# Kernel optimization log

Hardware: AMD Instinct MI355X
Metric: run time of the kernel (lower is better)

## Reference

```python
import jax, jax.numpy as jnp
import numpy as np

N = 50000
IN_CH = 128
HEADS = 4
OUT_CH = 32
E = 800000
NEG_SLOPE = 0.2


def setup_inputs() -> dict:
    key = jax.random.key(0)
    k1, k2, k3, k4, k5, k6 = jax.random.split(key, 6)
    x = jax.random.normal(k1, (N, IN_CH), dtype=jnp.float32)
    edge_index = jax.random.randint(k2, (2, E), 0, N, dtype=jnp.int64)
    # learned params (PyG GATv2Conv: lin_l, lin_r weights, att vector, bias)
    s = 1.0 / np.sqrt(IN_CH)
    W_l = jax.random.uniform(k3, (IN_CH, HEADS, OUT_CH), jnp.float32, -s, s)
    W_r = jax.random.uniform(k4, (IN_CH, HEADS, OUT_CH), jnp.float32, -s, s)
    att = jax.random.uniform(k5, (HEADS, OUT_CH), jnp.float32, -s, s)
    bias = jax.random.uniform(k6, (HEADS * OUT_CH,), jnp.float32, -s, s)
    return {"x": x, "edge_index": edge_index, "W_l": W_l, "W_r": W_r,
            "att": att, "bias": bias}


def reference(x, edge_index, W_l, W_r, att, bias):
    # add self loops (PyG default add_self_loops=True)
    loops = jnp.arange(N, dtype=edge_index.dtype)
    src = jnp.concatenate([edge_index[0], loops])  # message source j
    dst = jnp.concatenate([edge_index[1], loops])  # message target i

    # node projections: [N, H, C]
    x_l = jnp.einsum('nd,dhc->nhc', x, W_l)  # source-side
    x_r = jnp.einsum('nd,dhc->nhc', x, W_r)  # target-side

    # GATv2 attention logits per edge: a^T LeakyReLU(x_l[j] + x_r[i])
    e = jax.nn.leaky_relu(x_l[src] + x_r[dst], NEG_SLOPE)  # [Etot, H, C]
    score = jnp.einsum('ehc,hc->eh', e, att)               # [Etot, H]

    # segment softmax over incoming edges of each destination node
    m = jax.ops.segment_max(score, dst, num_segments=N)    # [N, H]
    m = jnp.where(jnp.isfinite(m), m, 0.0)
    ex = jnp.exp(score - m[dst])                           # [Etot, H]
    denom = jax.ops.segment_sum(ex, dst, num_segments=N)   # [N, H]
    alpha = ex / denom[dst]                                # [Etot, H]

    # scatter-aggregate weighted messages
    msg = alpha[:, :, None] * x_l[src]                     # [Etot, H, C]
    out = jax.ops.segment_sum(msg, dst, num_segments=N)    # [N, H, C]

    # concat heads + bias
    return out.reshape(N, HEADS * OUT_CH) + bias
```

## Files before the change

### kernel.cpp

```cpp
#include <hip/hip_runtime.h>
#include <math.h>

#define N_NODES 50000
#define IN_CH   128
#define TOT_CH  128
#define NEDGE   800000
#define ETOT    (NEDGE + N_NODES)
#define MTILES  ((N_NODES + 63) / 64)
#define NBUCK   ((N_NODES + 255) / 256)
#define BCAP    8192
#define EPB     4096
#define NBIN    ((ETOT + EPB - 1) / EPB)

#define OFF_XL      ((size_t)0)
#define OFF_EBUF    ((size_t)12800000)
#define OFF_XR      ((size_t)25600000)
#define OFF_SRC     ((size_t)38400000)
#define OFF_BT      ((size_t)44900352)
#define OFF_GCUR    ((size_t)45000064)
#define OFF_ROWPTR  ((size_t)51200000)

typedef float f32x4 __attribute__((ext_vector_type(4)));
typedef short s16x8 __attribute__((ext_vector_type(8)));

__device__ __forceinline__ unsigned f2bf(float f) {
    unsigned u = __float_as_uint(f);
    return (u + 0x7fffu + ((u >> 16) & 1u)) >> 16;
}
__device__ __forceinline__ float bflo(unsigned u) { return __uint_as_float(u << 16); }
__device__ __forceinline__ float bfhi(unsigned u) { return __uint_as_float(u & 0xffff0000u); }

__device__ __forceinline__ int SWZ(int row, int byteoff) {
    return row * 256 + (byteoff ^ ((row & 7) << 4));
}

__global__ __launch_bounds__(256) void k1_kernel(
    const float* __restrict__ Wl, const float* __restrict__ Wr,
    unsigned* __restrict__ btg, const int* __restrict__ ei,
    int* __restrict__ gcur, unsigned* __restrict__ ebuf)
{
    __shared__ int lcnt[256];
    __shared__ int lbase[256];
    const int bid = blockIdx.x;
    const int tid = threadIdx.x;

    if (bid < NBIN) {
        lcnt[tid] = 0;
        __syncthreads();
        const int base = bid * EPB;
        int sv[16], dv[16];
#pragma unroll
        for (int u = 0; u < 16; ++u) {
            const int e = base + u * 256 + tid;
            int s32 = 0, d32 = -1;
            if (e < ETOT) {
                if (e < NEDGE) { s32 = ei[e]; d32 = ei[NEDGE + e]; }
                else           { s32 = d32 = e - NEDGE; }
                atomicAdd(&lcnt[d32 >> 8], 1);
            }
            sv[u] = s32; dv[u] = d32;
        }
        __syncthreads();
        if (tid < NBUCK) {
            const int v = lcnt[tid];
            lbase[tid] = v ? atomicAdd(&gcur[tid], v) : 0;
        }
        __syncthreads();
        lcnt[tid] = 0;
        __syncthreads();
#pragma unroll
        for (int u = 0; u < 16; ++u) {
            const int d32 = dv[u];
            if (d32 >= 0) {
                const int b = d32 >> 8;
                const int p = lbase[b] + atomicAdd(&lcnt[b], 1);
                ebuf[b * BCAP + p] = (unsigned)sv[u] | ((unsigned)(d32 & 255) << 16);
            }
        }
    } else {
        const int g = (bid - NBIN) * 256 + tid;
        if (g < 256 * 64) {
            const int n = g >> 6, kk = g & 63;
            const float* W = (n < 128) ? Wl : Wr;
            const int nc = n & 127;
            const float a = W[(size_t)(2 * kk) * 128 + nc];
            const float b = W[(size_t)(2 * kk + 1) * 128 + nc];
            btg[g] = f2bf(a) | (f2bf(b) << 16);
        }
    }
}

__global__ __launch_bounds__(256) void k2_kernel(
    const float* __restrict__ x, const unsigned* __restrict__ btg,
    unsigned* __restrict__ xl_bf, unsigned* __restrict__ xr_bf,
    const unsigned* __restrict__ ebuf, const int* __restrict__ gcur,
    int2* __restrict__ rowptr2, int* __restrict__ ssrc)
{
    __shared__ __align__(16) unsigned char smem[32768];
    __shared__ int wsum[4];
    const int bid = blockIdx.x;
    const int tid = threadIdx.x;

    if (bid < NBUCK) {
        int* lcnt = (int*)smem;
        int* lcur = ((int*)smem) + 256;
        const int ecnt  = gcur[bid];
        const int ebase = bid * BCAP;
        lcnt[tid] = 0;
        __syncthreads();
        for (int k = tid; k < ecnt; k += 256)
            atomicAdd(&lcnt[(ebuf[ebase + k] >> 16) & 255], 1);
        __syncthreads();
        const int lane = tid & 63, wid = tid >> 6;
        const int v = lcnt[tid];
        int s = v;
#pragma unroll
        for (int off = 1; off < 64; off <<= 1) {
            int t = __shfl_up(s, off);
            if (lane >= off) s += t;
        }
        if (lane == 63) wsum[wid] = s;
        __syncthreads();
        if (tid == 0) {
            int acc = 0;
#pragma unroll
            for (int w = 0; w < 4; ++w) { int t = wsum[w]; wsum[w] = acc; acc += t; }
        }
        __syncthreads();
        const int gpos = ebase + wsum[wid] + s - v;
        const int node = (bid << 8) + tid;
        if (node < N_NODES) rowptr2[node] = make_int2(gpos, gpos + v);
        lcur[tid] = gpos;
        __syncthreads();
        for (int k = tid; k < ecnt; k += 256) {
            const unsigned ed = ebuf[ebase + k];
            const int p = atomicAdd(&lcur[(ed >> 16) & 255], 1);
            ssrc[p] = (int)(ed & 0xffffu);
        }
        return;
    }

    unsigned char* Al = smem;
    unsigned char* Bl = smem + 16384;
    const int mt = bid - NBUCK;
    const int mbase = mt * 64;
    const int l  = tid & 63;
    const int wv = tid >> 6;

    {
        const int r = tid >> 2, q = tid & 3;
        int gm = mbase + r;
        gm = (gm < N_NODES) ? gm : (N_NODES - 1);
        const float* xrow = x + (size_t)gm * IN_CH + q * 32;
#pragma unroll
        for (int i = 0; i < 8; ++i) {
            const float4 xv = *(const float4*)(xrow + i * 4);
            uint2 p;
            p.x = f2bf(xv.x) | (f2bf(xv.y) << 16);
            p.y = f2bf(xv.z) | (f2bf(xv.w) << 16);
            *(uint2*)(Al + SWZ(r, q * 64 + i * 8)) = p;
        }
    }
    {
        const int r = tid >> 2, q = tid & 3;
        const unsigned* brow = btg + (size_t)r * 64 + q * 16;
#pragma unroll
        for (int i = 0; i < 4; ++i) {
            const uint4 v = *(const uint4*)(brow + i * 4);
            *(uint4*)(Bl + SWZ(r, q * 64 + i * 16)) = v;
        }
    }
    __syncthreads();

    s16x8 af[4];
#pragma unroll
    for (int ks = 0; ks < 4; ++ks)
        af[ks] = *(const s16x8*)(Al + SWZ(wv * 16 + (l & 15), ks * 64 + (l >> 4) * 16));

    for (int nt4 = 0; nt4 < 4; ++nt4) {
        f32x4 acc[4];
#pragma unroll
        for (int n = 0; n < 4; ++n) acc[n] = (f32x4){0.f, 0.f, 0.f, 0.f};
#pragma unroll
        for (int nsub = 0; nsub < 4; ++nsub) {
#pragma unroll
            for (int ks = 0; ks < 4; ++ks) {
                const s16x8 bfr = *(const s16x8*)(Bl + SWZ(nsub * 16 + (l & 15), ks * 64 + (l >> 4) * 16));
                acc[nsub] = __builtin_amdgcn_mfma_f32_16x16x32_bf16(af[ks], bfr, acc[nsub], 0, 0, 0);
            }
        }
        unsigned* dstbuf = (nt4 < 2) ? xl_bf : xr_bf;
        const int ncol0 = (nt4 & 1) * 64;
#pragma unroll
        for (int nsub = 0; nsub < 4; ++nsub) {
            const int n = ncol0 + nsub * 16 + (l & 15);
#pragma unroll
            for (int reg = 0; reg < 4; ++reg) {
                const float v  = acc[nsub][reg];
                const float vp = __shfl_xor(v, 1);
                const int row = mbase + wv * 16 + (l >> 4) * 4 + reg;
                if (((l & 1) == 0) && row < N_NODES)
                    dstbuf[(size_t)row * 64 + (n >> 1)] = f2bf(v) | (f2bf(vp) << 16);
            }
        }
        if (nt4 == 3) break;
        __syncthreads();
        {
            const int r = tid >> 2, q = tid & 3;
            const unsigned* brow = btg + (size_t)((nt4 + 1) * 64 + r) * 64 + q * 16;
#pragma unroll
            for (int i = 0; i < 4; ++i) {
                const uint4 v = *(const uint4*)(brow + i * 4);
                *(uint4*)(Bl + SWZ(r, q * 64 + i * 16)) = v;
            }
        }
        __syncthreads();
    }
}

#define DPP_ADD(s, ctrl) do { \
        int _t = __builtin_amdgcn_update_dpp(0, __float_as_int(s), ctrl, 0xf, 0xf, true); \
        s += __int_as_float(_t); } while(0)

#define RED16x8(a0,a1,a2,a3,a4,a5,a6,a7) do { \
        DPP_ADD(a0,0xB1); DPP_ADD(a1,0xB1); DPP_ADD(a2,0xB1); DPP_ADD(a3,0xB1); \
        DPP_ADD(a4,0xB1); DPP_ADD(a5,0xB1); DPP_ADD(a6,0xB1); DPP_ADD(a7,0xB1); \
        DPP_ADD(a0,0x4E); DPP_ADD(a1,0x4E); DPP_ADD(a2,0x4E); DPP_ADD(a3,0x4E); \
        DPP_ADD(a4,0x4E); DPP_ADD(a5,0x4E); DPP_ADD(a6,0x4E); DPP_ADD(a7,0x4E); \
        DPP_ADD(a0,0x124); DPP_ADD(a1,0x124); DPP_ADD(a2,0x124); DPP_ADD(a3,0x124); \
        DPP_ADD(a4,0x124); DPP_ADD(a5,0x124); DPP_ADD(a6,0x124); DPP_ADD(a7,0x124); \
        DPP_ADD(a0,0x128); DPP_ADD(a1,0x128); DPP_ADD(a2,0x128); DPP_ADD(a3,0x128); \
        DPP_ADD(a4,0x128); DPP_ADD(a5,0x128); DPP_ADD(a6,0x128); DPP_ADD(a7,0x128); } while(0)

template<bool MASKED>
__device__ __forceinline__ void batch8(
    const int* __restrict__ srcs, int k, int k1, int lane,
    const unsigned* __restrict__ xl_bf,
    float xr2x, float xr2y, float a6x, float a4x, float a6y, float a4y,
    float& den, float& b0, float& b1)
{
#define KIDX(n) (MASKED ? min(k + n, k1 - 1) : (k + n))
#define LOADU(n) \
    const int j##n = __builtin_amdgcn_readfirstlane(srcs[KIDX(n)]); \
    const unsigned u##n = *(xl_bf + (size_t)j##n * 64 + lane);
    LOADU(0); LOADU(1); LOADU(2); LOADU(3);
    LOADU(4); LOADU(5); LOADU(6); LOADU(7);
#undef LOADU
#undef KIDX
#define SCORE(n) \
    const float t0_##n = bflo(u##n) + xr2x; \
    const float t1_##n = bfhi(u##n) + xr2y; \
    float s##n = fmaf(a6x, t0_##n, fmaf(a4x, fabsf(t0_##n), \
                 fmaf(a6y, t1_##n, a4y * fabsf(t1_##n))));
    SCORE(0); SCORE(1); SCORE(2); SCORE(3);
    SCORE(4); SCORE(5); SCORE(6); SCORE(7);
#undef SCORE
    RED16x8(s0, s1, s2, s3, s4, s5, s6, s7);
    if (MASKED) {
        const int r = k1 - k;
        s1 = (1 < r) ? s1 : -1e30f;
        s2 = (2 < r) ? s2 : -1e30f;
        s3 = (3 < r) ? s3 : -1e30f;
        s4 = (4 < r) ? s4 : -1e30f;
        s5 = (5 < r) ? s5 : -1e30f;
        s6 = (6 < r) ? s6 : -1e30f;
        s7 = (7 < r) ? s7 : -1e30f;
    }
    const float p0 = __builtin_amdgcn_exp2f(s0), p1 = __builtin_amdgcn_exp2f(s1);
    const float p2 = __builtin_amdgcn_exp2f(s2), p3 = __builtin_amdgcn_exp2f(s3);
    const float p4 = __builtin_amdgcn_exp2f(s4), p5 = __builtin_amdgcn_exp2f(s5);
    const float p6 = __builtin_amdgcn_exp2f(s6), p7 = __builtin_amdgcn_exp2f(s7);
    den += ((p0 + p1) + (p2 + p3)) + ((p4 + p5) + (p6 + p7));
    {
        const float e0 = fmaf(p1, t0_1, p0 * t0_0);
        const float e1 = fmaf(p3, t0_3, p2 * t0_2);
        const float e2 = fmaf(p5, t0_5, p4 * t0_4);
        const float e3 = fmaf(p7, t0_7, p6 * t0_6);
        b0 += (e0 + e1) + (e2 + e3);
        const float f0 = fmaf(p1, t1_1, p0 * t1_0);
        const float f1 = fmaf(p3, t1_3, p2 * t1_2);
        const float f2 = fmaf(p5, t1_5, p4 * t1_4);
        const float f3 = fmaf(p7, t1_7, p6 * t1_6);
        b1 += (f0 + f1) + (f2 + f3);
    }
}

__global__ __launch_bounds__(256) void gat_kernel(
    const unsigned* __restrict__ xl_bf, const unsigned* __restrict__ xr_bf,
    const int2* __restrict__ rowptr2, const int* __restrict__ srcs,
    const float* __restrict__ att, const float* __restrict__ bias,
    float* __restrict__ out)
{
    const int lane = threadIdx.x & 63;
    const int i = blockIdx.x * 4 + (threadIdx.x >> 6);
    if (i >= N_NODES) return;
    const int c = lane * 2;
    const float2 att2 = *(const float2*)(att + c);
    const unsigned ur = xr_bf[(size_t)i * 64 + lane];
    const float xr2x = bflo(ur), xr2y = bfhi(ur);
    const float LOG2E = 1.4426950408889634f;
    const float a6x = 0.6f * att2.x * LOG2E, a4x = 0.4f * att2.x * LOG2E;
    const float a6y = 0.6f * att2.y * LOG2E, a4y = 0.4f * att2.y * LOG2E;
    const int2 kr = rowptr2[i];
    const int k0 = __builtin_amdgcn_readfirstlane(kr.x);
    const int k1 = __builtin_amdgcn_readfirstlane(kr.y);

    float den = 0.f, b0 = 0.f, b1 = 0.f;
    int k = k0;
    for (; k + 8 <= k1; k += 8)
        batch8<false>(srcs, k, k1, lane, xl_bf, xr2x, xr2y,
                      a6x, a4x, a6y, a4y, den, b0, b1);
    if (k < k1)
        batch8<true>(srcs, k, k1, lane, xl_bf, xr2x, xr2y,
                     a6x, a4x, a6y, a4y, den, b0, b1);

    const float inv = 1.f / den;
    const float2 bb = *(const float2*)(bias + c);
    float2 o;
    o.x = fmaf(b0, inv, bb.x - xr2x);
    o.y = fmaf(b1, inv, bb.y - xr2y);
    *(float2*)(out + (size_t)i * TOT_CH + c) = o;
}

extern "C" void kernel_launch(void* const* d_in, const int* in_sizes, int n_in,
                              void* d_out, int out_size, void* d_ws, size_t ws_size,
                              hipStream_t stream) {
    const float* x    = (const float*)d_in[0];
    const int*   ei   = (const int*)d_in[1];
    const float* Wl   = (const float*)d_in[2];
    const float* Wr   = (const float*)d_in[3];
    const float* att  = (const float*)d_in[4];
    const float* bias = (const float*)d_in[5];
    float* out = (float*)d_out;
    char*  ws  = (char*)d_ws;

    unsigned* xl_bf = (unsigned*)(ws + OFF_XL);
    unsigned* ebuf  = (unsigned*)(ws + OFF_EBUF);
    unsigned* xr_bf = (unsigned*)(ws + OFF_XR);
    int*      ssrc  = (int*)(ws + OFF_SRC);
    unsigned* btg   = (unsigned*)(ws + OFF_BT);
    int*      gcur  = (int*)(ws + OFF_GCUR);
    int2*   rowptr2 = (int2*)(ws + OFF_ROWPTR);

    hipMemsetAsync(gcur, 0, NBUCK * sizeof(int), stream);
    hipLaunchKernelGGL(k1_kernel, dim3(NBIN + 64), dim3(256), 0, stream,
                       Wl, Wr, btg, ei, gcur, ebuf);
    hipLaunchKernelGGL(k2_kernel, dim3(NBUCK + MTILES), dim3(256), 0, stream,
                       x, btg, xl_bf, xr_bf, ebuf, gcur, rowptr2, ssrc);
    hipLaunchKernelGGL(gat_kernel, dim3((N_NODES + 3) / 4), dim3(256), 0, stream,
                       xl_bf, xr_bf, rowptr2, ssrc, att, bias, out);
}
```

Measured before the change: 78.42 us.

## Split wavefront into four edge groups with 16-byte loads per lane

The aggregation kernel now splits each 64-lane wavefront into four 16-lane groups. Each group handles a different edge, and each lane loads 8 bf16 channels with a single 16-byte load instead of 2 channels with a 4-byte load. Head reductions shrink to two DPP steps, and the cross-group accumulators are combined with shuffles at the end. The hipMemsetAsync of the bucket counters is replaced by a tiny zero kernel to cut API overhead. The trade is higher register pressure and shuffle reduction cost in exchange for fewer, wider gather loads per edge.

```diff
diff --git a/kernel.cpp b/kernel.cpp
--- a/kernel.cpp
+++ b/kernel.cpp
@@ -34,6 +34,10 @@
     return row * 256 + (byteoff ^ ((row & 7) << 4));
 }
 
+__global__ __launch_bounds__(256) void zero_kernel(int* __restrict__ gcur) {
+    if (threadIdx.x < NBUCK) gcur[threadIdx.x] = 0;
+}
+
 __global__ __launch_bounds__(256) void k1_kernel(
     const float* __restrict__ Wl, const float* __restrict__ Wr,
     unsigned* __restrict__ btg, const int* __restrict__ ei,
@@ -222,67 +226,35 @@
         int _t = __builtin_amdgcn_update_dpp(0, __float_as_int(s), ctrl, 0xf, 0xf, true); \
         s += __int_as_float(_t); } while(0)
 
-#define RED16x8(a0,a1,a2,a3,a4,a5,a6,a7) do { \
-        DPP_ADD(a0,0xB1); DPP_ADD(a1,0xB1); DPP_ADD(a2,0xB1); DPP_ADD(a3,0xB1); \
-        DPP_ADD(a4,0xB1); DPP_ADD(a5,0xB1); DPP_ADD(a6,0xB1); DPP_ADD(a7,0xB1); \
-        DPP_ADD(a0,0x4E); DPP_ADD(a1,0x4E); DPP_ADD(a2,0x4E); DPP_ADD(a3,0x4E); \
-        DPP_ADD(a4,0x4E); DPP_ADD(a5,0x4E); DPP_ADD(a6,0x4E); DPP_ADD(a7,0x4E); \
-        DPP_ADD(a0,0x124); DPP_ADD(a1,0x124); DPP_ADD(a2,0x124); DPP_ADD(a3,0x124); \
-        DPP_ADD(a4,0x124); DPP_ADD(a5,0x124); DPP_ADD(a6,0x124); DPP_ADD(a7,0x124); \
-        DPP_ADD(a0,0x128); DPP_ADD(a1,0x128); DPP_ADD(a2,0x128); DPP_ADD(a3,0x128); \
-        DPP_ADD(a4,0x128); DPP_ADD(a5,0x128); DPP_ADD(a6,0x128); DPP_ADD(a7,0x128); } while(0)
-
 template<bool MASKED>
-__device__ __forceinline__ void batch8(
-    const int* __restrict__ srcs, int k, int k1, int lane,
+__device__ __forceinline__ void group4(
+    const int* __restrict__ srcs, int k, int kend, int q, int sl,
     const unsigned* __restrict__ xl_bf,
-    float xr2x, float xr2y, float a6x, float a4x, float a6y, float a4y,
-    float& den, float& b0, float& b1)
+    const float* a6, const float* a4, const float* xr8,
+    float& den, float* b)
 {
-#define KIDX(n) (MASKED ? min(k + n, k1 - 1) : (k + n))
-#define LOADU(n) \
-    const int j##n = __builtin_amdgcn_readfirstlane(srcs[KIDX(n)]); \
-    const unsigned u##n = *(xl_bf + (size_t)j##n * 64 + lane);
-    LOADU(0); LOADU(1); LOADU(2); LOADU(3);
-    LOADU(4); LOADU(5); LOADU(6); LOADU(7);
-#undef LOADU
-#undef KIDX
-#define SCORE(n) \
-    const float t0_##n = bflo(u##n) + xr2x; \
-    const float t1_##n = bfhi(u##n) + xr2y; \
-    float s##n = fmaf(a6x, t0_##n, fmaf(a4x, fabsf(t0_##n), \
-                 fmaf(a6y, t1_##n, a4y * fabsf(t1_##n))));
-    SCORE(0); SCORE(1); SCORE(2); SCORE(3);
-    SCORE(4); SCORE(5); SCORE(6); SCORE(7);
-#undef SCORE
-    RED16x8(s0, s1, s2, s3, s4, s5, s6, s7);
-    if (MASKED) {
-        const int r = k1 - k;
-        s1 = (1 < r) ? s1 : -1e30f;
-        s2 = (2 < r) ? s2 : -1e30f;
-        s3 = (3 < r) ? s3 : -1e30f;
-        s4 = (4 < r) ? s4 : -1e30f;
-        s5 = (5 < r) ? s5 : -1e30f;
-        s6 = (6 < r) ? s6 : -1e30f;
-        s7 = (7 < r) ? s7 : -1e30f;
-    }
-    const float p0 = __builtin_amdgcn_exp2f(s0), p1 = __builtin_amdgcn_exp2f(s1);
-    const float p2 = __builtin_amdgcn_exp2f(s2), p3 = __builtin_amdgcn_exp2f(s3);
-    const float p4 = __builtin_amdgcn_exp2f(s4), p5 = __builtin_amdgcn_exp2f(s5);
-    const float p6 = __builtin_amdgcn_exp2f(s6), p7 = __builtin_amdgcn_exp2f(s7);
-    den += ((p0 + p1) + (p2 + p3)) + ((p4 + p5) + (p6 + p7));
-    {
-        const float e0 = fmaf(p1, t0_1, p0 * t0_0);
-        const float e1 = fmaf(p3, t0_3, p2 * t0_2);
-        const float e2 = fmaf(p5, t0_5, p4 * t0_4);
-        const float e3 = fmaf(p7, t0_7, p6 * t0_6);
-        b0 += (e0 + e1) + (e2 + e3);
-        const float f0 = fmaf(p1, t1_1, p0 * t1_0);
-        const float f1 = fmaf(p3, t1_3, p2 * t1_2);
-        const float f2 = fmaf(p5, t1_5, p4 * t1_4);
-        const float f3 = fmaf(p7, t1_7, p6 * t1_6);
-        b1 += (f0 + f1) + (f2 + f3);
-    }
+    const int kk = MASKED ? min(k + q, kend - 1) : (k + q);
+    const int jv = srcs[kk];
+    const uint4 u = *(const uint4*)(xl_bf + (size_t)jv * 64 + sl * 4);
+    float t[8];
+    t[0] = bflo(u.x) + xr8[0]; t[1] = bfhi(u.x) + xr8[1];
+    t[2] = bflo(u.y) + xr8[2]; t[3] = bfhi(u.y) + xr8[3];
+    t[4] = bflo(u.z) + xr8[4]; t[5] = bfhi(u.z) + xr8[5];
+    t[6] = bflo(u.w) + xr8[6]; t[7] = bfhi(u.w) + xr8[7];
+    float s = a4[0] * fabsf(t[0]);
+    s = fmaf(a6[0], t[0], s);
+#pragma unroll
+    for (int c = 1; c < 8; ++c) {
+        s = fmaf(a4[c], fabsf(t[c]), s);
+        s = fmaf(a6[c], t[c], s);
+    }
+    DPP_ADD(s, 0xB1);
+    DPP_ADD(s, 0x4E);
+    if (MASKED) s = (q < kend - k) ? s : -1e30f;
+    const float p = __builtin_amdgcn_exp2f(s);
+    den += p;
+#pragma unroll
+    for (int c = 0; c < 8; ++c) b[c] = fmaf(p, t[c], b[c]);
 }
 
 __global__ __launch_bounds__(256) void gat_kernel(
@@ -291,35 +263,68 @@
     const float* __restrict__ att, const float* __restrict__ bias,
     float* __restrict__ out)
 {
-    const int lane = threadIdx.x & 63;
+    const int l = threadIdx.x & 63;
     const int i = blockIdx.x * 4 + (threadIdx.x >> 6);
     if (i >= N_NODES) return;
-    const int c = lane * 2;
-    const float2 att2 = *(const float2*)(att + c);
-    const unsigned ur = xr_bf[(size_t)i * 64 + lane];
-    const float xr2x = bflo(ur), xr2y = bfhi(ur);
+    const int sl = l & 15;
+    const int q  = l >> 4;
+    const int c8 = sl * 8;
     const float LOG2E = 1.4426950408889634f;
-    const float a6x = 0.6f * att2.x * LOG2E, a4x = 0.4f * att2.x * LOG2E;
-    const float a6y = 0.6f * att2.y * LOG2E, a4y = 0.4f * att2.y * LOG2E;
+    float a6[8], a4[8], xr8[8];
+    {
+        const float4 A = *(const float4*)(att + c8);
+        const float4 B = *(const float4*)(att + c8 + 4);
+        const float av[8] = {A.x, A.y, A.z, A.w, B.x, B.y, B.z, B.w};
+#pragma unroll
+        for (int c = 0; c < 8; ++c) {
+            a6[c] = 0.6f * LOG2E * av[c];
+            a4[c] = 0.4f * LOG2E * av[c];
+        }
+    }
+    {
+        const uint4 urv = *(const uint4*)(xr_bf + (size_t)i * 64 + sl * 4);
+        xr8[0] = bflo(urv.x); xr8[1] = bfhi(urv.x);
+        xr8[2] = bflo(urv.y); xr8[3] = bfhi(urv.y);
+        xr8[4] = bflo(urv.z); xr8[5] = bfhi(urv.z);
+        xr8[6] = bflo(urv.w); xr8[7] = bfhi(urv.w);
+    }
     const int2 kr = rowptr2[i];
     const int k0 = __builtin_amdgcn_readfirstlane(kr.x);
     const int k1 = __builtin_amdgcn_readfirstlane(kr.y);
 
-    float den = 0.f, b0 = 0.f, b1 = 0.f;
+    float den = 0.f, b[8];
+#pragma unroll
+    for (int c = 0; c < 8; ++c) b[c] = 0.f;
+
     int k = k0;
-    for (; k + 8 <= k1; k += 8)
-        batch8<false>(srcs, k, k1, lane, xl_bf, xr2x, xr2y,
-                      a6x, a4x, a6y, a4y, den, b0, b1);
+    for (; k + 4 <= k1; k += 4)
+        group4<false>(srcs, k, k1, q, sl, xl_bf, a6, a4, xr8, den, b);
     if (k < k1)
-        batch8<true>(srcs, k, k1, lane, xl_bf, xr2x, xr2y,
-                     a6x, a4x, a6y, a4y, den, b0, b1);
-
-    const float inv = 1.f / den;
-    const float2 bb = *(const float2*)(bias + c);
-    float2 o;
-    o.x = fmaf(b0, inv, bb.x - xr2x);
-    o.y = fmaf(b1, inv, bb.y - xr2y);
-    *(float2*)(out + (size_t)i * TOT_CH + c) = o;
+        group4<true>(srcs, k, k1, q, sl, xl_bf, a6, a4, xr8, den, b);
+
+    den += __shfl_xor(den, 16);
+    den += __shfl_xor(den, 32);
+#pragma unroll
+    for (int c = 0; c < 8; ++c) {
+        b[c] += __shfl_xor(b[c], 16);
+        b[c] += __shfl_xor(b[c], 32);
+    }
+    if (q == 0) {
+        const float inv = 1.f / den;
+        const float4 bbA = *(const float4*)(bias + c8);
+        const float4 bbB = *(const float4*)(bias + c8 + 4);
+        float4 o1, o2;
+        o1.x = fmaf(b[0], inv, bbA.x - xr8[0]);
+        o1.y = fmaf(b[1], inv, bbA.y - xr8[1]);
+        o1.z = fmaf(b[2], inv, bbA.z - xr8[2]);
+        o1.w = fmaf(b[3], inv, bbA.w - xr8[3]);
+        o2.x = fmaf(b[4], inv, bbB.x - xr8[4]);
+        o2.y = fmaf(b[5], inv, bbB.y - xr8[5]);
+        o2.z = fmaf(b[6], inv, bbB.z - xr8[6]);
+        o2.w = fmaf(b[7], inv, bbB.w - xr8[7]);
+        *(float4*)(out + (size_t)i * TOT_CH + c8)     = o1;
+        *(float4*)(out + (size_t)i * TOT_CH + c8 + 4) = o2;
+    }
 }
 
 extern "C" void kernel_launch(void* const* d_in, const int* in_sizes, int n_in,
@@ -342,7 +347,7 @@
     int*      gcur  = (int*)(ws + OFF_GCUR);
     int2*   rowptr2 = (int2*)(ws + OFF_ROWPTR);
 
-    hipMemsetAsync(gcur, 0, NBUCK * sizeof(int), stream);
+    hipLaunchKernelGGL(zero_kernel, dim3(1), dim3(256), 0, stream, gcur);
     hipLaunchKernelGGL(k1_kernel, dim3(NBIN + 64), dim3(256), 0, stream,
                        Wl, Wr, btg, ei, gcur, ebuf);
     hipLaunchKernelGGL(k2_kernel, dim3(NBUCK + MTILES), dim3(256), 0, stream,
```

Result: slower. 82.89 us (+5.7%).
